# Kernel optimization log

Measured on AMD Instinct MI355X. Metric: run time of the kernel, lower is better.

## Reference

```python
import jax, jax.numpy as jnp
import numpy as np

N = 50000      # nodes
E = 800000     # edges (avg degree 16)
IN = 128       # in_feats
H = 8          # num_heads
EMB = 32       # attention embedding dim (mode != 'cross')
OUT = 16       # out_feats per head
EF = 7         # edge (bond) feature dim


def setup_inputs() -> dict:
    key = jax.random.key(0)
    ks = jax.random.split(key, 12)
    s = 0.05  # xavier-ish scale
    return {
        "feat": jax.random.normal(ks[0], (N, IN), jnp.float32),
        "bond": jax.random.uniform(ks[1], (E, EF), jnp.float32),
        "src": jax.random.randint(ks[2], (E,), 0, N, jnp.int32),
        "dst": jax.random.randint(ks[3], (E,), 0, N, jnp.int32),
        "Wq": jax.random.normal(ks[4], (IN, H * EMB), jnp.float32) * s,
        "Wk": jax.random.normal(ks[5], (IN, H * EMB), jnp.float32) * s,
        "Wv": jax.random.normal(ks[6], (IN, H * OUT), jnp.float32) * s,
        "Wek": jax.random.normal(ks[7], (EF, H * EMB), jnp.float32) * s,
        "bek": jnp.zeros((H * EMB,), jnp.float32),
        "Wefc": jax.random.normal(ks[8], (EF, H * OUT), jnp.float32) * s,
        "befc": jnp.zeros((H * OUT,), jnp.float32),
        "bias": jnp.zeros((H * OUT,), jnp.float32),
    }


def reference(feat, bond, src, dst, Wq, Wk, Wv, Wek, bek, Wefc, befc, bias):
    n = feat.shape[0]
    # node projections
    q = (feat @ Wq).reshape(n, H, EMB)      # query
    k = (feat @ Wk).reshape(n, H, EMB)      # key
    v = (feat @ Wv).reshape(n, H, OUT)      # ft (values)
    # per-edge key from bond features
    ek = (bond @ Wek + bek).reshape(-1, H, EMB)
    # mode 'add': e = sum((q[u] + k[v]) * edge_key) over embedding dim  -> [E, H]
    e = ((q[src] + k[dst]) * ek).sum(axis=-1)
    # edge_softmax: segment softmax over incoming edges per destination node
    m = jax.ops.segment_max(e, dst, num_segments=n)          # [N, H]
    ex = jnp.exp(e - m[dst])
    denom = jax.ops.segment_sum(ex, dst, num_segments=n)     # [N, H]
    a = ex / denom[dst]                                      # [E, H]
    # per-edge feature projection
    ef = (bond @ Wefc + befc).reshape(-1, H, OUT)
    # message = ft[src] * edge_feat * a, aggregated by sum at dst
    msg = v[src] * ef * a[:, :, None]                        # [E, H, OUT]
    rst = jax.ops.segment_sum(msg, dst, num_segments=n)      # [N, H, OUT]
    rst = rst + bias.reshape(1, H, OUT)
    return rst
```

## Files before the change

### kernel.cpp

```cpp
#include <hip/hip_runtime.h>
#include <hip/hip_bf16.h>

#define HD   8
#define EMBD 32
#define OUTF 16
#define EFD  7
#define INFD 128
#define QKD  256
#define VOD  128
#define GQD  64
#define CAPMAX 96
#define GPB  8
#define PSTR 100

typedef __attribute__((ext_vector_type(8))) short short8;
typedef __attribute__((ext_vector_type(4))) float f32x4;

__device__ __forceinline__ float b2f(unsigned short u) {
    return __uint_as_float(((unsigned int)u) << 16);
}
__device__ __forceinline__ unsigned short f2b(float f) {
    __hip_bfloat16 h = __float2bfloat16(f);
    return __builtin_bit_cast(unsigned short, h);
}

__global__ __launch_bounds__(256) void setup_kernel(
    const float* __restrict__ Wq, const float* __restrict__ Wk,
    const float* __restrict__ Wv, const float* __restrict__ Wek,
    const float* __restrict__ bek, unsigned short* __restrict__ GwT,
    int* __restrict__ counts, int N)
{
    if (blockIdx.x != 0) {
        int i = (blockIdx.x - 1) * 256 + threadIdx.x;
        int stride = (gridDim.x - 1) * 256;
        for (; i < N; i += stride) counts[i] = 0;
        return;
    }
    __shared__ float sWek[EFD * QKD];
    __shared__ float sbek[QKD];
    const int t = threadIdx.x;
    for (int i = t; i < EFD * QKD; i += 256) sWek[i] = Wek[i];
    for (int i = t; i < QKD; i += 256) sbek[i] = bek[i];
    __syncthreads();

    for (int p = t; p < 2048; p += 256) {
        int side = p >> 10;
        int r = (p >> 3) & 127;
        int h = p & 7;
        const float* W = side ? Wk : Wq;
        float wrow[EMBD];
        #pragma unroll
        for (int d = 0; d < EMBD; d++) wrow[d] = W[(size_t)r * QKD + h * EMBD + d];
        #pragma unroll
        for (int f = 0; f < EFD; f++) {
            float m = 0.f;
            #pragma unroll
            for (int d = 0; d < EMBD; d++) m += wrow[d] * sWek[f * QKD + h * EMBD + d];
            GwT[(size_t)(side * 64 + h * 8 + f) * 128 + r] = f2b(m);
        }
        float mb = 0.f;
        #pragma unroll
        for (int d = 0; d < EMBD; d++) mb += wrow[d] * sbek[h * EMBD + d];
        GwT[(size_t)(side * 64 + h * 8 + 7) * 128 + r] = f2b(mb);
    }
    for (int i = t; i < INFD * VOD; i += 256) {
        int r = i >> 7, c = i & 127;
        GwT[(size_t)(128 + c) * 128 + r] = f2b(Wv[(size_t)r * VOD + c]);
    }
}

__global__ __launch_bounds__(256) void work_kernel(
    const float* __restrict__ feat, const unsigned short* __restrict__ GwT,
    unsigned short* __restrict__ gq, unsigned short* __restrict__ gk,
    unsigned short* __restrict__ v_bf, int M,
    const int* __restrict__ src, const int* __restrict__ dst,
    const float* __restrict__ bond, int E,
    int* __restrict__ counts, short8* __restrict__ edata, int cap, int pg)
{
    if ((int)blockIdx.x >= pg) {
        int i = (blockIdx.x - pg) * 256 + threadIdx.x;
        int stride = (gridDim.x - pg) * 256;
        for (; i < E; i += stride) {
            int d = dst[i];
            const float* bp = bond + (size_t)i * EFD;
            short8 rec;
            rec[0] = (short)(unsigned short)src[i];
            #pragma unroll
            for (int f = 0; f < EFD; f++) rec[1 + f] = (short)f2b(bp[f]);
            int p = atomicAdd(&counts[d], 1);
            if (p < cap) edata[(size_t)d * cap + p] = rec;
        }
        return;
    }
    const int wave = threadIdx.x >> 6, lane = threadIdx.x & 63;
    const int quad = lane >> 4, l16 = lane & 15;
    const int m0 = blockIdx.x * 64 + wave * 16;
    const int mrow = m0 + l16;
    const int arow = (mrow < M) ? mrow : 0;

    f32x4 acc[16];
    #pragma unroll
    for (int ct = 0; ct < 16; ct++) acc[ct] = (f32x4){0.f, 0.f, 0.f, 0.f};

    #pragma unroll
    for (int ks = 0; ks < 4; ks++) {
        const float* fp = feat + (size_t)arow * INFD + ks * 32 + quad * 8;
        float4 f0 = *(const float4*)(fp);
        float4 f1 = *(const float4*)(fp + 4);
        short8 a;
        a[0] = (short)f2b(f0.x); a[1] = (short)f2b(f0.y);
        a[2] = (short)f2b(f0.z); a[3] = (short)f2b(f0.w);
        a[4] = (short)f2b(f1.x); a[5] = (short)f2b(f1.y);
        a[6] = (short)f2b(f1.z); a[7] = (short)f2b(f1.w);
        #pragma unroll
        for (int ct = 0; ct < 16; ct++) {
            short8 b = *(const short8*)(GwT + (size_t)(ct * 16 + l16) * 128 + ks * 32 + quad * 8);
            acc[ct] = __builtin_amdgcn_mfma_f32_16x16x32_bf16(a, b, acc[ct], 0, 0, 0);
        }
    }

    const int mt = m0 + quad * 4;
    #pragma unroll
    for (int ct = 0; ct < 16; ct++) {
        int nn = ct * 16 + l16;
        unsigned short* outp; int nc, ldo;
        if (ct < 4)      { outp = gq;   nc = nn;       ldo = GQD; }
        else if (ct < 8) { outp = gk;   nc = nn - 64;  ldo = GQD; }
        else             { outp = v_bf; nc = nn - 128; ldo = VOD; }
        #pragma unroll
        for (int r = 0; r < 4; r++) {
            int mm = mt + r;
            if (mm < M) outp[(size_t)mm * ldo + nc] = f2b(acc[ct][r]);
        }
    }
}

__global__ __launch_bounds__(128) void aggregate_kernel(
    const short8* __restrict__ edata,
    const unsigned short* __restrict__ gq,
    const unsigned short* __restrict__ gk,
    const unsigned short* __restrict__ v_bf,
    const int* __restrict__ counts,
    const float* __restrict__ Wefc,
    const float* __restrict__ befc,
    const float* __restrict__ bias,
    float* __restrict__ out, int N, int cap)
{
    __shared__ float sP[8 * PSTR];
    __shared__ float sB[CAPMAX][8];
    __shared__ int   sS[CAPMAX];

    const int t = threadIdx.x;
    const int h = t >> 4;
    const int lh = t & 7;

    float wef[EFD];
    #pragma unroll
    for (int f = 0; f < EFD; f++) wef[f] = Wefc[f * VOD + t];
    const float bef  = befc[t];
    const float bout = bias[t];

    for (int g = 0; g < GPB; g++) {
        const int n = blockIdx.x * GPB + g;
        if (n >= N) break;
        const int cnt = min(counts[n], cap);

        float gkl[8];
        {
            short8 gv = *(const short8*)(gk + (size_t)n * GQD + lh * 8);
            #pragma unroll
            for (int j = 0; j < 8; j++) gkl[j] = b2f((unsigned short)gv[j]);
        }

        for (int i = t; i < cnt; i += 128) {
            short8 r = edata[(size_t)n * cap + i];
            sS[i] = (int)(unsigned short)r[0];
            float4 b0 = make_float4(b2f((unsigned short)r[1]), b2f((unsigned short)r[2]),
                                    b2f((unsigned short)r[3]), b2f((unsigned short)r[4]));
            float4 b1 = make_float4(b2f((unsigned short)r[5]), b2f((unsigned short)r[6]),
                                    b2f((unsigned short)r[7]), 0.f);
            *(float4*)&sB[i][0] = b0;
            *(float4*)&sB[i][4] = b1;
        }
        __syncthreads();

        for (int idx = t; idx < cnt * 8; idx += 128) {
            int el = idx >> 3;
            short8 gv = *(const short8*)(gq + (size_t)sS[el] * GQD + lh * 8);
            float4 b0 = *(const float4*)&sB[el][0];
            float4 b1 = *(const float4*)&sB[el][4];
            float lv = b2f((unsigned short)gv[7]) + gkl[7];
            lv += b0.x * (b2f((unsigned short)gv[0]) + gkl[0]);
            lv += b0.y * (b2f((unsigned short)gv[1]) + gkl[1]);
            lv += b0.z * (b2f((unsigned short)gv[2]) + gkl[2]);
            lv += b0.w * (b2f((unsigned short)gv[3]) + gkl[3]);
            lv += b1.x * (b2f((unsigned short)gv[4]) + gkl[4]);
            lv += b1.y * (b2f((unsigned short)gv[5]) + gkl[5]);
            lv += b1.z * (b2f((unsigned short)gv[6]) + gkl[6]);
            sP[lh * PSTR + el] = __expf(lv);
        }
        __syncthreads();

        float acc = 0.f, l = 0.f;
        int e = 0;
        for (; e + 4 <= cnt; e += 4) {
            float4 pv = *(const float4*)&sP[h * PSTR + e];
            int s0 = sS[e], s1 = sS[e + 1], s2 = sS[e + 2], s3 = sS[e + 3];
            float v0 = b2f(v_bf[(size_t)s0 * VOD + t]);
            float v1 = b2f(v_bf[(size_t)s1 * VOD + t]);
            float v2 = b2f(v_bf[(size_t)s2 * VOD + t]);
            float v3 = b2f(v_bf[(size_t)s3 * VOD + t]);
            float vv[4] = {v0, v1, v2, v3};
            float pp[4] = {pv.x, pv.y, pv.z, pv.w};
            #pragma unroll
            for (int j = 0; j < 4; j++) {
                float4 b0 = *(const float4*)&sB[e + j][0];
                float4 b1 = *(const float4*)&sB[e + j][4];
                float ef = bef + b0.x * wef[0] + b0.y * wef[1] + b0.z * wef[2]
                         + b0.w * wef[3] + b1.x * wef[4] + b1.y * wef[5] + b1.z * wef[6];
                acc += pp[j] * ef * vv[j];
                l += pp[j];
            }
        }
        for (; e < cnt; e++) {
            float p = sP[h * PSTR + e];
            float4 b0 = *(const float4*)&sB[e][0];
            float4 b1 = *(const float4*)&sB[e][4];
            float ef = bef + b0.x * wef[0] + b0.y * wef[1] + b0.z * wef[2]
                     + b0.w * wef[3] + b1.x * wef[4] + b1.y * wef[5] + b1.z * wef[6];
            float vv = b2f(v_bf[(size_t)sS[e] * VOD + t]);
            acc += p * ef * vv;
            l += p;
        }
        const float inv = (l > 0.f) ? 1.f / l : 0.f;
        out[(size_t)n * VOD + t] = acc * inv + bout;
        __syncthreads();
    }
}

extern "C" void kernel_launch(void* const* d_in, const int* in_sizes, int n_in,
                              void* d_out, int out_size, void* d_ws, size_t ws_size,
                              hipStream_t stream) {
    const float* feat = (const float*)d_in[0];
    const float* bond = (const float*)d_in[1];
    const int* src  = (const int*)d_in[2];
    const int* dst  = (const int*)d_in[3];
    const float* Wq   = (const float*)d_in[4];
    const float* Wk   = (const float*)d_in[5];
    const float* Wv   = (const float*)d_in[6];
    const float* Wek  = (const float*)d_in[7];
    const float* bek  = (const float*)d_in[8];
    const float* Wefc = (const float*)d_in[9];
    const float* befc = (const float*)d_in[10];
    const float* bias = (const float*)d_in[11];

    const int N = in_sizes[0] / INFD;
    const int E = in_sizes[2];

    size_t off = 0;
    auto carve = [&](size_t bytes) -> void* {
        void* p = (char*)d_ws + off;
        off += (bytes + 255) & ~(size_t)255;
        return p;
    };
    unsigned short* GwT  = (unsigned short*)carve((size_t)256 * 128 * 2);
    unsigned short* gq   = (unsigned short*)carve((size_t)N * GQD * 2);
    unsigned short* gk   = (unsigned short*)carve((size_t)N * GQD * 2);
    unsigned short* v_bf = (unsigned short*)carve((size_t)N * VOD * 2);
    int* counts    = (int*)carve((size_t)N * 4);

    size_t remain = (ws_size > off) ? (ws_size - off) : 0;
    int cap = (int)(remain / ((size_t)N * 16));
    if (cap > 64) cap = 64;
    if (cap > CAPMAX) cap = CAPMAX;
    if (cap < 1) cap = 1;
    short8* edata = (short8*)carve((size_t)N * cap * 16);

    setup_kernel<<<65, 256, 0, stream>>>(Wq, Wk, Wv, Wek, bek, GwT, counts, N);

    const int pg = (N + 63) / 64;
    work_kernel<<<pg + 3072, 256, 0, stream>>>(feat, GwT, gq, gk, v_bf, N,
                                               src, dst, bond, E, counts, edata, cap, pg);

    aggregate_kernel<<<(N + GPB - 1) / GPB, VOD, 0, stream>>>(
        edata, gq, gk, v_bf, counts, Wefc, befc, bias, (float*)d_out, N, cap);
}
```

Measured before the change: 300.1 us.

## Compute edge-feature projection with MFMA and restructure aggregation per wave

The aggregate kernel now computes the per-edge feature projection (bond @ Wefc + befc) with 16x16x32 bf16 MFMA tiles, with the bias folded in through a constant-one column. Bond features stay in shared memory as bf16 instead of being expanded to fp32. The softmax denominator moves to a separate shuffle reduction. Each wave handles four heads and reduces partial sums across lane groups. CAPMAX shrinks from 96 to 64, which silently truncates any node with more in-edges than that, and the edge projection is now done in bf16.

```diff
diff --git a/kernel.cpp b/kernel.cpp
--- a/kernel.cpp
+++ b/kernel.cpp
@@ -9,9 +9,9 @@
 #define QKD  256
 #define VOD  128
 #define GQD  64
-#define CAPMAX 96
+#define CAPMAX 64
 #define GPB  8
-#define PSTR 100
+#define PSTR 68
 
 typedef __attribute__((ext_vector_type(8))) short short8;
 typedef __attribute__((ext_vector_type(4))) float f32x4;
@@ -146,94 +146,125 @@
     const float* __restrict__ bias,
     float* __restrict__ out, int N, int cap)
 {
-    __shared__ float sP[8 * PSTR];
-    __shared__ float sB[CAPMAX][8];
-    __shared__ int   sS[CAPMAX];
-
-    const int t = threadIdx.x;
-    const int h = t >> 4;
+    __shared__ __align__(16) float sP[8 * PSTR];
+    __shared__ __align__(16) unsigned short sBond[CAPMAX][8];
+    __shared__ __align__(16) int sS[CAPMAX];
+    __shared__ float sL[8];
+
+    const int t  = threadIdx.x;
     const int lh = t & 7;
-
-    float wef[EFD];
+    const int wv = t >> 6;
+    const int l  = t & 63;
+    const int lrow = l & 15;
+    const int lhi  = l >> 4;
+    const int cbase = wv * 64 + lrow;
+
+    short8 Bfr[4]; float bout[4];
     #pragma unroll
-    for (int f = 0; f < EFD; f++) wef[f] = Wefc[f * VOD + t];
-    const float bef  = befc[t];
-    const float bout = bias[t];
+    for (int nt = 0; nt < 4; nt++) {
+        short8 b = {0,0,0,0,0,0,0,0};
+        float bo = 0.f;
+        if (lhi == 0) {
+            const int c = cbase + nt * 16;
+            #pragma unroll
+            for (int f = 0; f < EFD; f++) b[f] = (short)f2b(Wefc[f * VOD + c]);
+            b[7] = (short)f2b(befc[c]);
+            bo = bias[c];
+        }
+        Bfr[nt] = b; bout[nt] = bo;
+    }
 
     for (int g = 0; g < GPB; g++) {
         const int n = blockIdx.x * GPB + g;
         if (n >= N) break;
         const int cnt = min(counts[n], cap);
+        const int r16 = (cnt + 15) & ~15;
+        const int Mtiles = r16 >> 4;
 
         float gkl[8];
         {
-            short8 gv = *(const short8*)(gk + (size_t)n * GQD + lh * 8);
+            short8 gv = *(const short8*)(gk + (unsigned)n * GQD + lh * 8);
             #pragma unroll
             for (int j = 0; j < 8; j++) gkl[j] = b2f((unsigned short)gv[j]);
         }
 
-        for (int i = t; i < cnt; i += 128) {
-            short8 r = edata[(size_t)n * cap + i];
-            sS[i] = (int)(unsigned short)r[0];
-            float4 b0 = make_float4(b2f((unsigned short)r[1]), b2f((unsigned short)r[2]),
-                                    b2f((unsigned short)r[3]), b2f((unsigned short)r[4]));
-            float4 b1 = make_float4(b2f((unsigned short)r[5]), b2f((unsigned short)r[6]),
-                                    b2f((unsigned short)r[7]), 0.f);
-            *(float4*)&sB[i][0] = b0;
-            *(float4*)&sB[i][4] = b1;
+        for (int i = t; i < r16; i += 128) {
+            short8 st = {0,0,0,0,0,0,0,0};
+            int sv = 0;
+            if (i < cnt) {
+                short8 r = edata[(size_t)n * cap + i];
+                sv = (int)(unsigned short)r[0];
+                #pragma unroll
+                for (int f = 0; f < EFD; f++) st[f] = r[1 + f];
+                st[7] = (short)0x3F80;
+            }
+            sS[i] = sv;
+            *(short8*)&sBond[i][0] = st;
         }
         __syncthreads();
 
-        for (int idx = t; idx < cnt * 8; idx += 128) {
-            int el = idx >> 3;
-            short8 gv = *(const short8*)(gq + (size_t)sS[el] * GQD + lh * 8);
-            float4 b0 = *(const float4*)&sB[el][0];
-            float4 b1 = *(const float4*)&sB[el][4];
-            float lv = b2f((unsigned short)gv[7]) + gkl[7];
-            lv += b0.x * (b2f((unsigned short)gv[0]) + gkl[0]);
-            lv += b0.y * (b2f((unsigned short)gv[1]) + gkl[1]);
-            lv += b0.z * (b2f((unsigned short)gv[2]) + gkl[2]);
-            lv += b0.w * (b2f((unsigned short)gv[3]) + gkl[3]);
-            lv += b1.x * (b2f((unsigned short)gv[4]) + gkl[4]);
-            lv += b1.y * (b2f((unsigned short)gv[5]) + gkl[5]);
-            lv += b1.z * (b2f((unsigned short)gv[6]) + gkl[6]);
-            sP[lh * PSTR + el] = __expf(lv);
+        for (int idx = t; idx < r16 * 8; idx += 128) {
+            const int el = idx >> 3;
+            float ex = 0.f;
+            if (el < cnt) {
+                short8 gv = *(const short8*)(gq + (unsigned)sS[el] * GQD + lh * 8);
+                short8 bb = *(const short8*)&sBond[el][0];
+                float lv = b2f((unsigned short)gv[7]) + gkl[7];
+                #pragma unroll
+                for (int f = 0; f < EFD; f++)
+                    lv += b2f((unsigned short)bb[f]) * (b2f((unsigned short)gv[f]) + gkl[f]);
+                ex = __expf(lv);
+            }
+            sP[lh * PSTR + el] = ex;
         }
         __syncthreads();
 
-        float acc = 0.f, l = 0.f;
-        int e = 0;
-        for (; e + 4 <= cnt; e += 4) {
-            float4 pv = *(const float4*)&sP[h * PSTR + e];
-            int s0 = sS[e], s1 = sS[e + 1], s2 = sS[e + 2], s3 = sS[e + 3];
-            float v0 = b2f(v_bf[(size_t)s0 * VOD + t]);
-            float v1 = b2f(v_bf[(size_t)s1 * VOD + t]);
-            float v2 = b2f(v_bf[(size_t)s2 * VOD + t]);
-            float v3 = b2f(v_bf[(size_t)s3 * VOD + t]);
-            float vv[4] = {v0, v1, v2, v3};
-            float pp[4] = {pv.x, pv.y, pv.z, pv.w};
-            #pragma unroll
-            for (int j = 0; j < 4; j++) {
-                float4 b0 = *(const float4*)&sB[e + j][0];
-                float4 b1 = *(const float4*)&sB[e + j][4];
-                float ef = bef + b0.x * wef[0] + b0.y * wef[1] + b0.z * wef[2]
-                         + b0.w * wef[3] + b1.x * wef[4] + b1.y * wef[5] + b1.z * wef[6];
-                acc += pp[j] * ef * vv[j];
-                l += pp[j];
+        if (t < 64) {
+            const int h8 = t >> 3, sub = t & 7;
+            float part = 0.f;
+            for (int e = sub; e < cnt; e += 8) part += sP[h8 * PSTR + e];
+            part += __shfl_xor(part, 1, 64);
+            part += __shfl_xor(part, 2, 64);
+            part += __shfl_xor(part, 4, 64);
+            if (sub == 0) sL[h8] = part;
+        }
+
+        float accw[4] = {0.f, 0.f, 0.f, 0.f};
+        for (int mt = 0; mt < Mtiles; mt++) {
+            short8 A = {0,0,0,0,0,0,0,0};
+            if (lhi == 0) A = *(const short8*)&sBond[mt * 16 + lrow][0];
+            const int e0 = mt * 16 + lhi * 4;
+            const int4 ss = *(const int4*)&sS[e0];
+            #pragma unroll
+            for (int nt = 0; nt < 4; nt++) {
+                f32x4 C = __builtin_amdgcn_mfma_f32_16x16x32_bf16(
+                    A, Bfr[nt], (f32x4){0.f, 0.f, 0.f, 0.f}, 0, 0, 0);
+                const int h = wv * 4 + nt;
+                const int c = cbase + nt * 16;
+                const float4 pv = *(const float4*)&sP[h * PSTR + e0];
+                const float v0 = b2f(v_bf[(unsigned)(ss.x * VOD + c)]);
+                const float v1 = b2f(v_bf[(unsigned)(ss.y * VOD + c)]);
+                const float v2 = b2f(v_bf[(unsigned)(ss.z * VOD + c)]);
+                const float v3 = b2f(v_bf[(unsigned)(ss.w * VOD + c)]);
+                accw[nt] = fmaf(pv.x * C[0], v0, accw[nt]);
+                accw[nt] = fmaf(pv.y * C[1], v1, accw[nt]);
+                accw[nt] = fmaf(pv.z * C[2], v2, accw[nt]);
+                accw[nt] = fmaf(pv.w * C[3], v3, accw[nt]);
             }
         }
-        for (; e < cnt; e++) {
-            float p = sP[h * PSTR + e];
-            float4 b0 = *(const float4*)&sB[e][0];
-            float4 b1 = *(const float4*)&sB[e][4];
-            float ef = bef + b0.x * wef[0] + b0.y * wef[1] + b0.z * wef[2]
-                     + b0.w * wef[3] + b1.x * wef[4] + b1.y * wef[5] + b1.z * wef[6];
-            float vv = b2f(v_bf[(size_t)sS[e] * VOD + t]);
-            acc += p * ef * vv;
-            l += p;
-        }
-        const float inv = (l > 0.f) ? 1.f / l : 0.f;
-        out[(size_t)n * VOD + t] = acc * inv + bout;
+        __syncthreads();
+
+        #pragma unroll
+        for (int nt = 0; nt < 4; nt++) {
+            float s = accw[nt];
+            s += __shfl_xor(s, 16, 64);
+            s += __shfl_xor(s, 32, 64);
+            if (lhi == 0) {
+                const float L = sL[wv * 4 + nt];
+                const float iv = (L > 0.f) ? 1.f / L : 0.f;
+                out[(size_t)n * VOD + cbase + nt * 16] = s * iv + bout[nt];
+            }
+        }
         __syncthreads();
     }
 }
```

Result: slower. 312.0 us (+3.9%).
